# Performance work log

Hardware: AMD Instinct MI355X
Metric: run time of the kernel (lower is better)

Reference implementation:

```python
import jax, jax.numpy as jnp
import numpy as np

COLOR_CODE_NUMBER = 9

def _conv(x, w, b):
    # NCHW conv, 3x3, stride 1, padding 1 (SAME)
    y = jax.lax.conv_general_dilated(x, w, (1, 1), 'SAME',
                                     dimension_numbers=('NCHW', 'OIHW', 'NCHW'))
    return y + b[None, :, None, None]

def setup_inputs() -> dict:
    key = jax.random.key(0)
    ks = jax.random.split(key, 10)
    C, H, W = 256, 256, 256
    ms = 32
    s = 0.02
    x = jax.random.normal(ks[0], (1, C, H, W), dtype=jnp.float32)
    masks = jax.random.randint(ks[1], (COLOR_CODE_NUMBER, H, W), 0, 2, dtype=jnp.int32)
    w1 = jax.random.normal(ks[2], (128, 256, 3, 3), dtype=jnp.float32) * s
    b1 = jnp.zeros((128,), jnp.float32)
    w2 = jax.random.normal(ks[3], (64, 128, 3, 3), dtype=jnp.float32) * s
    b2 = jnp.zeros((64,), jnp.float32)
    w3 = jax.random.normal(ks[4], (ms, 64, 3, 3), dtype=jnp.float32) * s
    b3 = jnp.zeros((ms,), jnp.float32)
    fc_w = jax.random.normal(ks[5], (ms * ms, ms * ms), dtype=jnp.float32) * s
    fc_b = jnp.zeros((ms * ms,), jnp.float32)
    return {'x': x, 'masks': masks, 'w1': w1, 'b1': b1, 'w2': w2, 'b2': b2,
            'w3': w3, 'b3': b3, 'fc_w': fc_w, 'fc_b': fc_b}

def reference(x, masks, w1, b1, w2, b2, w3, b3, fc_w, fc_b):
    xb, xc, xh, xw = x.shape
    N = xh * xw
    K = masks.shape[0]
    xv = x.reshape(xc, N)                       # [C, N]
    m = masks.reshape(K, N)                     # [K, N] int
    fg = (m > 0).astype(x.dtype)                # [K, N]
    counts = fg.sum(axis=1)                     # [K]
    valid = counts >= 10.0                      # sum(mask) >= 10 for binary masks
    # per-mask gather -> mean-subtract -> scatter (sequential: later masks overwrite)
    fsm = xv
    for i in range(min(COLOR_CODE_NUMBER, K)):
        mean = (xv * fg[i]).sum(axis=1) / jnp.maximum(counts[i], 1.0)   # [C]
        sub = jnp.where(fg[i][None, :] > 0, xv - mean[:, None], fsm)
        fsm = jnp.where(valid[i], sub, fsm)
    # conv stack on mean-subtracted feature
    feat = fsm.reshape(xb, xc, xh, xw)
    feat = jax.nn.relu(_conv(feat, w1, b1))
    feat = jax.nn.relu(_conv(feat, w2, b2))
    feat = _conv(feat, w3, b3)                  # [1, ms, H, W]
    c = feat.shape[1]
    fv = feat.reshape(c, N)                     # [ms, N]
    # per-mask covariance + fc (vectorized over the 9 masks)
    fg1 = (m == 1).astype(feat.dtype)           # [K, N]
    cnt1 = fg1.sum(axis=1)                      # [K]
    masked = fv[None, :, :] * fg1[:, None, :]   # [K, ms, N]
    cov = jnp.einsum('kcn,kdn->kcd', masked, masked) / jnp.maximum(cnt1, 1.0)[:, None, None]
    trans = cov.reshape(K, c * c) @ fc_w.T + fc_b[None, :]              # [K, ms*ms]
    trans = jnp.where((cnt1 >= 10.0)[:, None], trans, jnp.zeros_like(trans))
    return trans, fsm
```

## Files before the change

### kernel.cpp

```cpp
#include <hip/hip_runtime.h>
#include <stdint.h>

#define N_PIX 65536
#define KM 9

typedef __bf16  bf16x8 __attribute__((ext_vector_type(8)));
typedef float   f32x4  __attribute__((ext_vector_type(4)));

__device__ __forceinline__ unsigned short f2bf(float f) {
    uint32_t u = __builtin_bit_cast(uint32_t, f);
    uint32_t r = (u + 0x7FFFu + ((u >> 16) & 1u)) >> 16;
    return (unsigned short)r;
}

#define WS_BITS  0u
#define WS_CNT   262144u
#define WS_CNT1  262208u
#define WS_SUMS  262272u
#define WS_MEANS 271488u
#define WS_W1T   282624u
#define WS_W2T   872448u
#define WS_W3T   1019904u
#define WS_COV   1056768u
#define WS_XB    2097152u
#define WS_FV    2097152u
#define WS_PART  14680064u
#define WS_C1B   35651584u
#define WS_C2B   52428800u

__global__ void k_pack(const int* __restrict__ masks, uint32_t* __restrict__ bits,
                       int* __restrict__ counts, int* __restrict__ cnt1) {
    int n = blockIdx.x * 256 + threadIdx.x;
    uint32_t fg = 0, f1 = 0;
#pragma unroll
    for (int k = 0; k < KM; ++k) {
        int m = masks[k * N_PIX + n];
        fg |= (uint32_t)(m > 0) << k;
        f1 |= (uint32_t)(m == 1) << k;
    }
    bits[n] = fg | (f1 << 16);
#pragma unroll
    for (int k = 0; k < KM; ++k) {
        unsigned long long b0 = __ballot((fg >> k) & 1);
        unsigned long long b1 = __ballot((f1 >> k) & 1);
        if ((threadIdx.x & 63) == 0) {
            atomicAdd(&counts[k], __popcll(b0));
            atomicAdd(&cnt1[k], __popcll(b1));
        }
    }
}

__global__ void k_sums(const float* __restrict__ x, const uint32_t* __restrict__ bits,
                       float* __restrict__ sums) {
    int c = blockIdx.x >> 4;
    int base = (blockIdx.x & 15) * 4096;
    float acc[KM];
#pragma unroll
    for (int k = 0; k < KM; ++k) acc[k] = 0.0f;
    const float* xc = x + (size_t)c * N_PIX;
    for (int i = 0; i < 16; ++i) {
        int px = base + i * 256 + threadIdx.x;
        float xv = xc[px];
        uint32_t b = bits[px];
#pragma unroll
        for (int k = 0; k < KM; ++k) acc[k] += ((b >> k) & 1) ? xv : 0.0f;
    }
#pragma unroll
    for (int k = 0; k < KM; ++k) {
        float v = acc[k];
        for (int off = 32; off; off >>= 1) v += __shfl_down(v, off);
        if ((threadIdx.x & 63) == 0) atomicAdd(&sums[k * 256 + c], v);
    }
}

__global__ void k_means(const float* __restrict__ sums, const int* __restrict__ counts,
                        float* __restrict__ means) {
    int k = blockIdx.x, c = threadIdx.x;
    means[k * 256 + c] = sums[k * 256 + c] / fmaxf((float)counts[k], 1.0f);
}

__global__ void k_fsm(const float* __restrict__ x, const uint32_t* __restrict__ bits,
                      const int* __restrict__ counts, const float* __restrict__ means,
                      float* __restrict__ fsm, unsigned short* __restrict__ xb) {
    __shared__ float mst[256 * 12];
    int tid = threadIdx.x;
    for (int t = tid; t < KM * 256; t += 256) {
        int k = t >> 8, c = t & 255;
        mst[c * 12 + k] = means[t];
    }
    __syncthreads();
    uint32_t vm = 0;
#pragma unroll
    for (int k = 0; k < KM; ++k) vm |= (uint32_t)(counts[k] >= 10) << k;
    int px = blockIdx.x * 256 + tid;
    int c0 = blockIdx.y * 128;
    uint32_t sel = bits[px] & vm & 0x1FFu;
    int kl = 0; float have = 0.0f;
    if (sel) { kl = 31 - __clz((int)sel); have = 1.0f; }
    for (int cb = 0; cb < 128; cb += 8) {
        int c = c0 + cb;
        uint32_t pk[4];
#pragma unroll
        for (int j = 0; j < 8; j += 2) {
            float v0 = x[(size_t)(c + j) * N_PIX + px]     - have * mst[(c + j) * 12 + kl];
            float v1 = x[(size_t)(c + j + 1) * N_PIX + px] - have * mst[(c + j + 1) * 12 + kl];
            fsm[(size_t)(c + j) * N_PIX + px] = v0;
            fsm[(size_t)(c + j + 1) * N_PIX + px] = v1;
            pk[j >> 1] = (uint32_t)f2bf(v0) | ((uint32_t)f2bf(v1) << 16);
        }
        uint4 w; w.x = pk[0]; w.y = pk[1]; w.z = pk[2]; w.w = pk[3];
        *(uint4*)&xb[(size_t)px * 256 + c] = w;
    }
}

__global__ void k_wpack(const float* __restrict__ w, unsigned short* __restrict__ wt,
                        int total, int OC, int IC) {
    int idx = blockIdx.x * 256 + threadIdx.x;
    if (idx >= total) return;
    int oc = idx / IC, ic = idx - oc * IC;
    const float* src = w + (size_t)idx * 9;
#pragma unroll
    for (int t = 0; t < 9; ++t)
        wt[((size_t)t * OC + oc) * IC + ic] = f2bf(src[t]);
}

template<int IC, int OC, bool RELU, bool F32OUT>
__global__ __launch_bounds__(256) void k_convm(const unsigned short* __restrict__ xin,
                                               const unsigned short* __restrict__ wt,
                                               const float* __restrict__ bias,
                                               unsigned short* __restrict__ ybf,
                                               float* __restrict__ yf) {
    constexpr int NT = OC / 16;
    constexpr int NC = IC / 32;
    __shared__ unsigned short xs[4 * 3 * 130 * 8];
    const int tid  = threadIdx.x;
    const int lane = tid & 63;
    const int wv   = tid >> 6;
    const int lo   = lane & 15;
    const int kg   = lane >> 4;
    const int y0   = blockIdx.x >> 1;
    const int x0   = (blockIdx.x & 1) << 7;

    f32x4 acc[2][NT];
#pragma unroll
    for (int m = 0; m < 2; ++m)
#pragma unroll
        for (int n = 0; n < NT; ++n) acc[m][n] = (f32x4){0.f, 0.f, 0.f, 0.f};
    float bs[NT];
#pragma unroll
    for (int n = 0; n < NT; ++n) bs[n] = bias[n * 16 + lo];

    for (int icc = 0; icc < NC; ++icc) {
        if (icc) __syncthreads();
        for (int u = tid; u < 1560; u += 256) {
            int row = u / 520;
            int r2  = u - row * 520;
            int px  = r2 >> 2;
            int icg = r2 & 3;
            int gy = y0 + row - 1;
            int gx = x0 + px - 1;
            uint4 v = make_uint4(0u, 0u, 0u, 0u);
            if ((unsigned)gy < 256u && (unsigned)gx < 256u)
                v = *(const uint4*)(xin + ((size_t)(gy * 256 + gx)) * IC + icc * 32 + icg * 8);
            *(uint4*)(xs + ((icg * 3 + row) * 130 + px) * 8) = v;
        }
        __syncthreads();
        const int abase = (kg * 3 * 130 + wv * 32 + lo) * 8;
#pragma unroll
        for (int tap = 0; tap < 9; ++tap) {
            const int tr = tap / 3, tc = tap % 3;
            bf16x8 wfrag[NT];
#pragma unroll
            for (int n = 0; n < NT; ++n)
                wfrag[n] = __builtin_bit_cast(bf16x8,
                    *(const uint4*)(wt + ((size_t)tap * OC + n * 16 + lo) * IC + icc * 32 + kg * 8));
            bf16x8 a0 = __builtin_bit_cast(bf16x8, *(const uint4*)(xs + abase + (tr * 130 + tc) * 8));
            bf16x8 a1 = __builtin_bit_cast(bf16x8, *(const uint4*)(xs + abase + (tr * 130 + tc) * 8 + 128));
#pragma unroll
            for (int n = 0; n < NT; ++n) {
                acc[0][n] = __builtin_amdgcn_mfma_f32_16x16x32_bf16(a0, wfrag[n], acc[0][n], 0, 0, 0);
                acc[1][n] = __builtin_amdgcn_mfma_f32_16x16x32_bf16(a1, wfrag[n], acc[1][n], 0, 0, 0);
            }
        }
    }
#pragma unroll
    for (int m = 0; m < 2; ++m) {
        int pxl = wv * 32 + m * 16 + kg * 4;
#pragma unroll
        for (int n = 0; n < NT; ++n) {
            int oc = n * 16 + lo;
#pragma unroll
            for (int r = 0; r < 4; ++r) {
                float v = acc[m][n][r] + bs[n];
                if (RELU) v = fmaxf(v, 0.0f);
                size_t px = (size_t)(y0 * 256 + x0 + pxl + r);
                if (F32OUT) yf[px * OC + oc] = v;
                else        ybf[px * OC + oc] = f2bf(v);
            }
        }
    }
}

__global__ __launch_bounds__(256) void k_cov(const float* __restrict__ fv,
                                             const uint32_t* __restrict__ bits,
                                             float* __restrict__ part) {
    __shared__ float sf[32 * 257];
    __shared__ uint32_t sb[256];
    int px0 = blockIdx.x * 256;
    int tid = threadIdx.x;
    const float4* src = (const float4*)(fv + (size_t)(px0 + tid) * 32);
#pragma unroll
    for (int q = 0; q < 8; ++q) {
        float4 v = src[q];
        sf[(q * 4 + 0) * 257 + tid] = v.x;
        sf[(q * 4 + 1) * 257 + tid] = v.y;
        sf[(q * 4 + 2) * 257 + tid] = v.z;
        sf[(q * 4 + 3) * 257 + tid] = v.w;
    }
    sb[tid] = bits[px0 + tid] >> 16;
    __syncthreads();
    int c = tid >> 3;
    int d4 = (tid & 7) * 4;
    float a[KM][4];
#pragma unroll
    for (int k = 0; k < KM; ++k)
#pragma unroll
        for (int j = 0; j < 4; ++j) a[k][j] = 0.0f;
#pragma unroll 2
    for (int px = 0; px < 256; ++px) {
        float fc = sf[c * 257 + px];
        float f0 = sf[(d4 + 0) * 257 + px];
        float f1 = sf[(d4 + 1) * 257 + px];
        float f2 = sf[(d4 + 2) * 257 + px];
        float f3 = sf[(d4 + 3) * 257 + px];
        uint32_t b = sb[px];
#pragma unroll
        for (int k = 0; k < KM; ++k) {
            float fm = ((b >> k) & 1) ? fc : 0.0f;
            a[k][0] = fmaf(fm, f0, a[k][0]);
            a[k][1] = fmaf(fm, f1, a[k][1]);
            a[k][2] = fmaf(fm, f2, a[k][2]);
            a[k][3] = fmaf(fm, f3, a[k][3]);
        }
    }
    float* po = part + (size_t)blockIdx.x * 9216 + (c * 32 + d4);
#pragma unroll
    for (int k = 0; k < KM; ++k)
#pragma unroll
        for (int j = 0; j < 4; ++j) po[k * 1024 + j] = a[k][j];
}

__global__ void k_covred(const float* __restrict__ part, float* __restrict__ cov) {
    int p = blockIdx.x * 256 + threadIdx.x;
    float s = 0.0f;
    for (int b = 0; b < 256; ++b) s += part[(size_t)b * 9216 + p];
    cov[p] = s;
}

__global__ void k_fc(const float* __restrict__ cov, const int* __restrict__ cnt1,
                     const float* __restrict__ fcw, const float* __restrict__ fcb,
                     float* __restrict__ trans) {
    int k = blockIdx.x;
    int j = blockIdx.y * 256 + threadIdx.x;
    __shared__ float sc[1024];
    int c1 = cnt1[k];
    float inv = 1.0f / fmaxf((float)c1, 1.0f);
    for (int t = threadIdx.x; t < 1024; t += 256) sc[t] = cov[k * 1024 + t] * inv;
    __syncthreads();
    const float4* wrow = (const float4*)(fcw + (size_t)j * 1024);
    float acc = fcb[j];
#pragma unroll 4
    for (int i4 = 0; i4 < 256; ++i4) {
        float4 wv = wrow[i4];
        acc += sc[i4 * 4 + 0] * wv.x + sc[i4 * 4 + 1] * wv.y +
               sc[i4 * 4 + 2] * wv.z + sc[i4 * 4 + 3] * wv.w;
    }
    trans[k * 1024 + j] = (c1 >= 10) ? acc : 0.0f;
}

extern "C" void kernel_launch(void* const* d_in, const int* in_sizes, int n_in,
                              void* d_out, int out_size, void* d_ws, size_t ws_size,
                              hipStream_t stream) {
    const float* x     = (const float*)d_in[0];
    const int*   masks = (const int*)  d_in[1];
    const float* w1    = (const float*)d_in[2];
    const float* b1    = (const float*)d_in[3];
    const float* w2    = (const float*)d_in[4];
    const float* b2    = (const float*)d_in[5];
    const float* w3    = (const float*)d_in[6];
    const float* b3    = (const float*)d_in[7];
    const float* fcw   = (const float*)d_in[8];
    const float* fcb   = (const float*)d_in[9];

    float* out   = (float*)d_out;
    float* trans = out;
    float* fsm   = out + KM * 1024;

    char* ws = (char*)d_ws;
    uint32_t* bits = (uint32_t*)(ws + WS_BITS);
    int*   counts  = (int*)  (ws + WS_CNT);
    int*   cnt1    = (int*)  (ws + WS_CNT1);
    float* sums    = (float*)(ws + WS_SUMS);
    float* means   = (float*)(ws + WS_MEANS);
    unsigned short* w1t = (unsigned short*)(ws + WS_W1T);
    unsigned short* w2t = (unsigned short*)(ws + WS_W2T);
    unsigned short* w3t = (unsigned short*)(ws + WS_W3T);
    float* cov     = (float*)(ws + WS_COV);
    unsigned short* xb  = (unsigned short*)(ws + WS_XB);
    float* fv      = (float*)(ws + WS_FV);
    float* part    = (float*)(ws + WS_PART);
    unsigned short* c1b = (unsigned short*)(ws + WS_C1B);
    unsigned short* c2b = (unsigned short*)(ws + WS_C2B);

    hipMemsetAsync(ws + WS_CNT, 0, 64 + 64 + 9216, stream);

    k_wpack<<<128, 256, 0, stream>>>(w1, w1t, 128 * 256, 128, 256);
    k_wpack<<< 32, 256, 0, stream>>>(w2, w2t,  64 * 128,  64, 128);
    k_wpack<<<  8, 256, 0, stream>>>(w3, w3t,  32 *  64,  32,  64);

    k_pack <<<256, 256, 0, stream>>>(masks, bits, counts, cnt1);
    k_sums <<<4096, 256, 0, stream>>>(x, bits, sums);
    k_means<<<KM, 256, 0, stream>>>(sums, counts, means);
    k_fsm  <<<dim3(256, 2), 256, 0, stream>>>(x, bits, counts, means, fsm, xb);

    k_convm<256, 128, true,  false><<<512, 256, 0, stream>>>(xb,  w1t, b1, c1b, nullptr);
    k_convm<128,  64, true,  false><<<512, 256, 0, stream>>>(c1b, w2t, b2, c2b, nullptr);
    k_convm< 64,  32, false, true ><<<512, 256, 0, stream>>>(c2b, w3t, b3, nullptr, fv);

    k_cov   <<<256, 256, 0, stream>>>(fv, bits, part);
    k_covred<<<36, 256, 0, stream>>>(part, cov);
    k_fc    <<<dim3(KM, 4), 256, 0, stream>>>(cov, cnt1, fcw, fcb, trans);
}
```

Baseline: 654.9 us.

## Pad conv activations with zero ring, prefetch input tiles via registers, retile conv1

Convolution inputs now live in 258x258 zero-padded NHWC buffers whose border is cleared by small ring kernels, so the conv tile loader no longer needs bounds checks. The conv kernel precomputes per-lane load offsets, double-buffers the next input-channel chunk in registers while MFMAs run, and loads all nine taps of weights up front. Tile shapes are templated, and conv1 now splits output channels across waves over 64-pixel blocks with twice as many workgroups. The cost is more registers for the weight fragments and staged loads, which may lower occupancy, plus extra launches and a slightly larger footprint for the padded buffers.

```diff
diff --git a/kernel.cpp b/kernel.cpp
--- a/kernel.cpp
+++ b/kernel.cpp
@@ -6,11 +6,12 @@
 
 typedef __bf16  bf16x8 __attribute__((ext_vector_type(8)));
 typedef float   f32x4  __attribute__((ext_vector_type(4)));
-
-__device__ __forceinline__ unsigned short f2bf(float f) {
+typedef unsigned short ushort;
+
+__device__ __forceinline__ ushort f2bf(float f) {
     uint32_t u = __builtin_bit_cast(uint32_t, f);
     uint32_t r = (u + 0x7FFFu + ((u >> 16) & 1u)) >> 16;
-    return (unsigned short)r;
+    return (ushort)r;
 }
 
 #define WS_BITS  0u
@@ -22,11 +23,25 @@
 #define WS_W2T   872448u
 #define WS_W3T   1019904u
 #define WS_COV   1056768u
-#define WS_XB    2097152u
+#define WS_XPAD  2097152u
 #define WS_FV    2097152u
-#define WS_PART  14680064u
-#define WS_C1B   35651584u
-#define WS_C2B   52428800u
+#define WS_PART  12582912u
+#define WS_C1PAD 36173824u
+#define WS_C2PAD 53212160u
+
+template<int C>
+__global__ void k_ring(ushort* p) {
+    constexpr int CU = C / 2;
+    int i = blockIdx.x * 256 + threadIdx.x;
+    if (i >= 1028 * CU) return;
+    int c = i % CU, px = i / CU;
+    int row, col;
+    if      (px < 258) { row = 0;   col = px; }
+    else if (px < 516) { row = 257; col = px - 258; }
+    else if (px < 772) { row = px - 516 + 1; col = 0; }
+    else               { row = px - 772 + 1; col = 257; }
+    ((uint32_t*)p)[(row * 258 + col) * CU + c] = 0u;
+}
 
 __global__ void k_pack(const int* __restrict__ masks, uint32_t* __restrict__ bits,
                        int* __restrict__ counts, int* __restrict__ cnt1) {
@@ -81,7 +96,7 @@
 
 __global__ void k_fsm(const float* __restrict__ x, const uint32_t* __restrict__ bits,
                       const int* __restrict__ counts, const float* __restrict__ means,
-                      float* __restrict__ fsm, unsigned short* __restrict__ xb) {
+                      float* __restrict__ fsm, ushort* __restrict__ xpad) {
     __shared__ float mst[256 * 12];
     int tid = threadIdx.x;
     for (int t = tid; t < KM * 256; t += 256) {
@@ -97,6 +112,8 @@
     uint32_t sel = bits[px] & vm & 0x1FFu;
     int kl = 0; float have = 0.0f;
     if (sel) { kl = 31 - __clz((int)sel); have = 1.0f; }
+    int y = px >> 8, xx = px & 255;
+    size_t pbase = ((size_t)(y + 1) * 258 + (xx + 1)) * 256;
     for (int cb = 0; cb < 128; cb += 8) {
         int c = c0 + cb;
         uint32_t pk[4];
@@ -109,11 +126,11 @@
             pk[j >> 1] = (uint32_t)f2bf(v0) | ((uint32_t)f2bf(v1) << 16);
         }
         uint4 w; w.x = pk[0]; w.y = pk[1]; w.z = pk[2]; w.w = pk[3];
-        *(uint4*)&xb[(size_t)px * 256 + c] = w;
-    }
-}
-
-__global__ void k_wpack(const float* __restrict__ w, unsigned short* __restrict__ wt,
+        *(uint4*)&xpad[pbase + c] = w;
+    }
+}
+
+__global__ void k_wpack(const float* __restrict__ w, ushort* __restrict__ wt,
                         int total, int OC, int IC) {
     int idx = blockIdx.x * 256 + threadIdx.x;
     if (idx >= total) return;
@@ -124,22 +141,45 @@
         wt[((size_t)t * OC + oc) * IC + ic] = f2bf(src[t]);
 }
 
-template<int IC, int OC, bool RELU, bool F32OUT>
-__global__ __launch_bounds__(256) void k_convm(const unsigned short* __restrict__ xin,
-                                               const unsigned short* __restrict__ wt,
+template<int IC, int OC, int NT, int PXG, bool RELU, bool F32OUT>
+__global__ __launch_bounds__(256) void k_convm(const ushort* __restrict__ xin,
+                                               const ushort* __restrict__ wt,
                                                const float* __restrict__ bias,
-                                               unsigned short* __restrict__ ybf,
+                                               ushort* __restrict__ ypad,
                                                float* __restrict__ yf) {
-    constexpr int NT = OC / 16;
-    constexpr int NC = IC / 32;
-    __shared__ unsigned short xs[4 * 3 * 130 * 8];
-    const int tid  = threadIdx.x;
-    const int lane = tid & 63;
-    const int wv   = tid >> 6;
-    const int lo   = lane & 15;
-    const int kg   = lane >> 4;
-    const int y0   = blockIdx.x >> 1;
-    const int x0   = (blockIdx.x & 1) << 7;
+    constexpr int NC   = IC / 32;
+    constexpr int BPX  = 32 * PXG;
+    constexpr int SEG  = 256 / BPX;
+    constexpr int PXP  = BPX + 2;
+    constexpr int RW   = PXP * 4;
+    constexpr int UNITS = 3 * RW;
+    constexpr int NCH  = (UNITS + 63) / 64;
+    constexpr int NV   = (NCH + 3) / 4;
+    static_assert(OC == 16 * NT * (4 / PXG), "tile mismatch");
+
+    __shared__ ushort xs[NCH * 512];
+
+    const int tid = threadIdx.x, lane = tid & 63, wv = tid >> 6;
+    const int lo = lane & 15, kg = lane >> 4;
+    const int y0 = blockIdx.x / SEG;
+    const int x0 = (blockIdx.x % SEG) * BPX;
+    const int wvpx = (wv % PXG) * 32;
+    const int oc0  = (wv / PXG) * 16 * NT;
+
+    uint32_t voff[NV];
+#pragma unroll
+    for (int j = 0; j < NV; ++j) {
+        int ch = wv + j * 4;
+        int u = ch * 64 + lane;
+        u = (u < UNITS) ? u : (UNITS - 1);
+        int row = u / RW;
+        int rem = u - row * RW;
+        int px = rem >> 2, icg = rem & 3;
+        voff[j] = (uint32_t)(((y0 + row) * 258 + (x0 + px)) * IC + icg * 8);
+    }
+
+    const ushort* wlane = wt + (size_t)(oc0 + lo) * IC + kg * 8;
+    const int abase = (wvpx + lo) * 32 + kg * 8;
 
     f32x4 acc[2][NT];
 #pragma unroll
@@ -148,54 +188,61 @@
         for (int n = 0; n < NT; ++n) acc[m][n] = (f32x4){0.f, 0.f, 0.f, 0.f};
     float bs[NT];
 #pragma unroll
-    for (int n = 0; n < NT; ++n) bs[n] = bias[n * 16 + lo];
+    for (int n = 0; n < NT; ++n) bs[n] = bias[oc0 + n * 16 + lo];
+
+    uint4 sreg[NV];
+#pragma unroll
+    for (int j = 0; j < NV; ++j)
+        if (wv + j * 4 < NCH) sreg[j] = *(const uint4*)(xin + voff[j]);
 
     for (int icc = 0; icc < NC; ++icc) {
-        if (icc) __syncthreads();
-        for (int u = tid; u < 1560; u += 256) {
-            int row = u / 520;
-            int r2  = u - row * 520;
-            int px  = r2 >> 2;
-            int icg = r2 & 3;
-            int gy = y0 + row - 1;
-            int gx = x0 + px - 1;
-            uint4 v = make_uint4(0u, 0u, 0u, 0u);
-            if ((unsigned)gy < 256u && (unsigned)gx < 256u)
-                v = *(const uint4*)(xin + ((size_t)(gy * 256 + gx)) * IC + icc * 32 + icg * 8);
-            *(uint4*)(xs + ((icg * 3 + row) * 130 + px) * 8) = v;
+#pragma unroll
+        for (int j = 0; j < NV; ++j) {
+            int ch = wv + j * 4;
+            if (ch < NCH) *(uint4*)(xs + ch * 512 + lane * 8) = sreg[j];
         }
         __syncthreads();
-        const int abase = (kg * 3 * 130 + wv * 32 + lo) * 8;
-#pragma unroll
-        for (int tap = 0; tap < 9; ++tap) {
-            const int tr = tap / 3, tc = tap % 3;
-            bf16x8 wfrag[NT];
+        bf16x8 wf[9][NT];
+#pragma unroll
+        for (int tap = 0; tap < 9; ++tap)
 #pragma unroll
             for (int n = 0; n < NT; ++n)
-                wfrag[n] = __builtin_bit_cast(bf16x8,
-                    *(const uint4*)(wt + ((size_t)tap * OC + n * 16 + lo) * IC + icc * 32 + kg * 8));
-            bf16x8 a0 = __builtin_bit_cast(bf16x8, *(const uint4*)(xs + abase + (tr * 130 + tc) * 8));
-            bf16x8 a1 = __builtin_bit_cast(bf16x8, *(const uint4*)(xs + abase + (tr * 130 + tc) * 8 + 128));
-#pragma unroll
-            for (int n = 0; n < NT; ++n) {
-                acc[0][n] = __builtin_amdgcn_mfma_f32_16x16x32_bf16(a0, wfrag[n], acc[0][n], 0, 0, 0);
-                acc[1][n] = __builtin_amdgcn_mfma_f32_16x16x32_bf16(a1, wfrag[n], acc[1][n], 0, 0, 0);
+                wf[tap][n] = __builtin_bit_cast(bf16x8,
+                    *(const uint4*)(wlane + ((size_t)tap * OC + n * 16) * IC + icc * 32));
+        if (icc + 1 < NC) {
+#pragma unroll
+            for (int j = 0; j < NV; ++j)
+                if (wv + j * 4 < NCH)
+                    sreg[j] = *(const uint4*)(xin + voff[j] + (icc + 1) * 32);
+        }
+#pragma unroll
+        for (int tr = 0; tr < 3; ++tr)
+#pragma unroll
+            for (int tc = 0; tc < 3; ++tc) {
+                bf16x8 a0 = __builtin_bit_cast(bf16x8,
+                    *(const uint4*)(xs + abase + (tr * PXP + tc) * 32));
+                bf16x8 a1 = __builtin_bit_cast(bf16x8,
+                    *(const uint4*)(xs + abase + (tr * PXP + tc) * 32 + 512));
+#pragma unroll
+                for (int n = 0; n < NT; ++n) {
+                    acc[0][n] = __builtin_amdgcn_mfma_f32_16x16x32_bf16(a0, wf[tr * 3 + tc][n], acc[0][n], 0, 0, 0);
+                    acc[1][n] = __builtin_amdgcn_mfma_f32_16x16x32_bf16(a1, wf[tr * 3 + tc][n], acc[1][n], 0, 0, 0);
+                }
             }
-        }
+        __syncthreads();
     }
 #pragma unroll
     for (int m = 0; m < 2; ++m) {
-        int pxl = wv * 32 + m * 16 + kg * 4;
+        int pxl = x0 + wvpx + m * 16 + kg * 4;
 #pragma unroll
         for (int n = 0; n < NT; ++n) {
-            int oc = n * 16 + lo;
+            int oc = oc0 + n * 16 + lo;
 #pragma unroll
             for (int r = 0; r < 4; ++r) {
                 float v = acc[m][n][r] + bs[n];
                 if (RELU) v = fmaxf(v, 0.0f);
-                size_t px = (size_t)(y0 * 256 + x0 + pxl + r);
-                if (F32OUT) yf[px * OC + oc] = v;
-                else        ybf[px * OC + oc] = f2bf(v);
+                if (F32OUT) yf[((size_t)y0 * 256 + pxl + r) * OC + oc] = v;
+                else        ypad[((size_t)(y0 + 1) * 258 + (pxl + r) + 1) * OC + oc] = f2bf(v);
             }
         }
     }
@@ -302,17 +349,21 @@
     int*   cnt1    = (int*)  (ws + WS_CNT1);
     float* sums    = (float*)(ws + WS_SUMS);
     float* means   = (float*)(ws + WS_MEANS);
-    unsigned short* w1t = (unsigned short*)(ws + WS_W1T);
-    unsigned short* w2t = (unsigned short*)(ws + WS_W2T);
-    unsigned short* w3t = (unsigned short*)(ws + WS_W3T);
+    ushort* w1t = (ushort*)(ws + WS_W1T);
+    ushort* w2t = (ushort*)(ws + WS_W2T);
+    ushort* w3t = (ushort*)(ws + WS_W3T);
     float* cov     = (float*)(ws + WS_COV);
-    unsigned short* xb  = (unsigned short*)(ws + WS_XB);
+    ushort* xpad  = (ushort*)(ws + WS_XPAD);
+    ushort* c1pad = (ushort*)(ws + WS_C1PAD);
+    ushort* c2pad = (ushort*)(ws + WS_C2PAD);
     float* fv      = (float*)(ws + WS_FV);
     float* part    = (float*)(ws + WS_PART);
-    unsigned short* c1b = (unsigned short*)(ws + WS_C1B);
-    unsigned short* c2b = (unsigned short*)(ws + WS_C2B);
 
     hipMemsetAsync(ws + WS_CNT, 0, 64 + 64 + 9216, stream);
+
+    k_ring<256><<<(1028 * 128 + 255) / 256, 256, 0, stream>>>(xpad);
+    k_ring<128><<<(1028 *  64 + 255) / 256, 256, 0, stream>>>(c1pad);
+    k_ring< 64><<<(1028 *  32 + 255) / 256, 256, 0, stream>>>(c2pad);
 
     k_wpack<<<128, 256, 0, stream>>>(w1, w1t, 128 * 256, 128, 256);
     k_wpack<<< 32, 256, 0, stream>>>(w2, w2t,  64 * 128,  64, 128);
@@ -321,11 +372,11 @@
     k_pack <<<256, 256, 0, stream>>>(masks, bits, counts, cnt1);
     k_sums <<<4096, 256, 0, stream>>>(x, bits, sums);
     k_means<<<KM, 256, 0, stream>>>(sums, counts, means);
-    k_fsm  <<<dim3(256, 2), 256, 0, stream>>>(x, bits, counts, means, fsm, xb);
-
-    k_convm<256, 128, true,  false><<<512, 256, 0, stream>>>(xb,  w1t, b1, c1b, nullptr);
-    k_convm<128,  64, true,  false><<<512, 256, 0, stream>>>(c1b, w2t, b2, c2b, nullptr);
-    k_convm< 64,  32, false, true ><<<512, 256, 0, stream>>>(c2b, w3t, b3, nullptr, fv);
+    k_fsm  <<<dim3(256, 2), 256, 0, stream>>>(x, bits, counts, means, fsm, xpad);
+
+    k_convm<256, 128, 4, 2, true,  false><<<1024, 256, 0, stream>>>(xpad,  w1t, b1, c1pad, nullptr);
+    k_convm<128,  64, 4, 4, true,  false><<< 512, 256, 0, stream>>>(c1pad, w2t, b2, c2pad, nullptr);
+    k_convm< 64,  32, 2, 4, false, true ><<< 512, 256, 0, stream>>>(c2pad, w3t, b3, nullptr, fv);
 
     k_cov   <<<256, 256, 0, stream>>>(fv, bits, part);
     k_covred<<<36, 256, 0, stream>>>(part, cov);
```

After: 705.6 us. +7.7%, slower.
